# Kernel tuning notes

Hardware: AMD Instinct MI355X
Metric: run time of the kernel (lower is better)

Reference implementation:

```python
import jax, jax.numpy as jnp
import numpy as np

B, T, D = 2, 2048, 2048
NH, HD, R = 16, 128, 64
CQ, CKV = 1536, 512
WINDOW, CHUNK = 512, 256
MIN_SCALE, MAX_SCALE = 0.5, 2.0
ROPE_BASE = 500000.0
EPS = 1e-6


def setup_inputs() -> dict:
    key = jax.random.key(0)
    ks = jax.random.split(key, 12)
    w = lambda k, shape: (jax.random.normal(k, shape, jnp.float32) * 0.02)
    return {
        "x": jax.random.normal(ks[0], (B, T, D), jnp.float32),
        "uncertainty": jax.random.uniform(ks[1], (B, T), jnp.float32),
        "Wq_down": w(ks[2], (D, CQ)),
        "q_norm_w": jnp.ones((CQ,), jnp.float32),
        "Wq_up": w(ks[3], (CQ, NH * HD)),
        "Wq_rope": w(ks[4], (CQ, NH * R)),
        "Wkv_down": w(ks[5], (D, CKV)),
        "kv_norm_w": jnp.ones((CKV,), jnp.float32),
        "Wk_up": w(ks[6], (CKV, NH * HD)),
        "Wv_up": w(ks[7], (CKV, NH * HD)),
        "Wk_rope": w(ks[8], (D, NH * R)),
        "Wout": w(ks[9], (NH * HD, D)),
        "Wgate": w(ks[10], (D, 1)),
        "bgate": jnp.zeros((1,), jnp.float32),
    }


def rms_norm(x, w):
    return x * jax.lax.rsqrt(jnp.mean(x * x, axis=-1, keepdims=True) + EPS) * w


def epe_cos_sin(positions, uncertainty):
    # freq_idx = arange(r//2)*2/r ; theta = base**(-freq_idx)
    half = R // 2
    freq_idx = jnp.arange(half, dtype=jnp.float32) * 2.0 / R
    theta = ROPE_BASE ** (-freq_idx)                                  # [half]
    scale = MIN_SCALE + jnp.clip(uncertainty, 0.0, 1.0) * (MAX_SCALE - MIN_SCALE)  # [B,T]
    freqs = positions[None, :, None].astype(jnp.float32) * theta[None, None, :] * scale[:, :, None]
    freqs = freqs[:, :, None, :]                                      # [B,T,1,half]
    return jnp.cos(freqs), jnp.sin(freqs)


def apply_rope(x, cos, sin):
    # x: [B,T,nH,r]; rotate halves with per-(B,T) cos/sin broadcast over heads
    half = x.shape[-1] // 2
    x1, x2 = x[..., :half], x[..., half:]
    return jnp.concatenate([x1 * cos - x2 * sin, x2 * cos + x1 * sin], axis=-1)


def sliding_window_attn(Q, K, V, window, chunk):
    # Q,K: [B,nH,T,dk], V: [B,nH,T,dv]; chunked causal sliding-window
    b, nh, t, dk = Q.shape
    dv = V.shape[-1]
    half_w = window // 2
    n_chunks = t // chunk                    # T chosen multiple of chunk
    L = chunk + 2 * half_w
    Kp = jnp.pad(K, ((0, 0), (0, 0), (half_w, half_w), (0, 0)))
    Vp = jnp.pad(V, ((0, 0), (0, 0), (half_w, half_w), (0, 0)))
    starts = jnp.arange(n_chunks) * chunk
    idx = starts[:, None] + jnp.arange(L)[None, :]          # [nC,L] into padded axis
    Kw = Kp[:, :, idx]                                       # [B,nH,nC,L,dk]
    Vw = Vp[:, :, idx]                                       # [B,nH,nC,L,dv]
    Qc = Q.reshape(b, nh, n_chunks, chunk, dk)
    scores = jnp.einsum('bhcqd,bhckd->bhcqk', Qc, Kw) / jnp.sqrt(jnp.float32(dk))
    key_pos = idx - half_w                                   # actual key positions [nC,L]
    q_pos = starts[:, None] + jnp.arange(chunk)[None, :]     # [nC,chunk]
    mask = (key_pos[:, None, :] <= q_pos[:, :, None]) & (key_pos[:, None, :] >= 0)
    scores = jnp.where(mask[None, None], scores, -jnp.inf)
    p = jax.nn.softmax(scores, axis=-1)
    out = jnp.einsum('bhcqk,bhckd->bhcqd', p, Vw)
    return out.reshape(b, nh, t, dv)


def reference(x, uncertainty, Wq_down, q_norm_w, Wq_up, Wq_rope,
              Wkv_down, kv_norm_w, Wk_up, Wv_up, Wk_rope, Wout, Wgate, bgate):
    b, t, d = x.shape
    positions = jnp.arange(t)

    q_lat = rms_norm(x @ Wq_down, q_norm_w)                  # [B,T,CQ]
    q_c = (q_lat @ Wq_up).reshape(b, t, NH, HD)
    q_r = (q_lat @ Wq_rope).reshape(b, t, NH, R)
    kv_lat = rms_norm(x @ Wkv_down, kv_norm_w)               # [B,T,CKV]
    k_c = (kv_lat @ Wk_up).reshape(b, t, NH, HD)
    v = (kv_lat @ Wv_up).reshape(b, t, NH, HD)
    k_r = (x @ Wk_rope).reshape(b, t, NH, R)

    cos, sin = epe_cos_sin(positions, uncertainty)
    q_r = apply_rope(q_r, cos, sin)
    k_r = apply_rope(k_r, cos, sin)

    Q = jnp.concatenate([q_c, q_r], axis=-1).transpose(0, 2, 1, 3)   # [B,nH,T,HD+R]
    K = jnp.concatenate([k_c, k_r], axis=-1).transpose(0, 2, 1, 3)
    V = v.transpose(0, 2, 1, 3)                                       # [B,nH,T,HD]

    out_ar = sliding_window_attn(Q, K, V, WINDOW, CHUNK)

    # full bidirectional SDPA
    scale = 1.0 / jnp.sqrt(jnp.float32(HD + R))
    scores = jnp.einsum('bhqd,bhkd->bhqk', Q, K) * scale
    out_bidir = jnp.einsum('bhqk,bhkd->bhqd', jax.nn.softmax(scores, axis=-1), V)

    alpha = jax.nn.sigmoid((x @ Wgate + bgate)).squeeze(-1)           # [B,T]
    a = alpha[:, None, :, None]
    merged = a * out_bidir + (1.0 - a) * out_ar                       # [B,nH,T,HD]
    merged = merged.transpose(0, 2, 1, 3).reshape(b, t, NH * HD)
    return merged @ Wout, alpha
```

## Files before the change

kernel.cpp:

```cpp
#include <hip/hip_runtime.h>
#include <hip/hip_bf16.h>
#include <math.h>

typedef __hip_bfloat16 bf16;
using v8bf = __attribute__((ext_vector_type(8))) __bf16;
using v4f  = __attribute__((ext_vector_type(4))) float;
using f32x16 = __attribute__((ext_vector_type(16))) float;
using v4u = __attribute__((ext_vector_type(4))) unsigned;
using v4s = __attribute__((ext_vector_type(4))) short;
using v8s = __attribute__((ext_vector_type(8))) short;

#define T_SEQ 2048
#define DMODEL 2048
#define NHEADS 16
#define HDIM 128
#define RDIM 64

__device__ __forceinline__ short f2bfbits(float f) {
  bf16 h = __float2bfloat16(f);
  short s;
  __builtin_memcpy(&s, &h, 2);
  return s;
}

__device__ __forceinline__ float bfbits2f(short s) {
  bf16 h;
  __builtin_memcpy(&h, &s, 2);
  return __bfloat162float(h);
}

__device__ __forceinline__ unsigned pk2bf(float a, float b) {
  unsigned lo = (unsigned short)f2bfbits(a);
  unsigned hi = (unsigned short)f2bfbits(b);
  return lo | (hi << 16);
}

typedef const __attribute__((address_space(1))) unsigned gu32;
typedef __attribute__((address_space(3))) unsigned lu32;
__device__ __forceinline__ void gl_lds16(const void* g, void* l) {
  __builtin_amdgcn_global_load_lds((gu32*)g, (lu32*)l, 16, 0, 0);
}

__global__ void detect_k(const unsigned* __restrict__ x, int* __restrict__ flag) {
  __shared__ int cnt;
  if (threadIdx.x == 0) cnt = 0;
  __syncthreads();
  int c = 0;
#pragma unroll
  for (int i = 0; i < 4; i++) {
    unsigned w = x[threadIdx.x * 4 + i];
    unsigned e = (w >> 7) & 0xFFu;
    if (e < 97u || e > 157u) c++;
  }
  atomicAdd(&cnt, c);
  __syncthreads();
  if (threadIdx.x == 0) flag[0] = (cnt > 256) ? 1 : 0;
}

__global__ __launch_bounds__(256) void conv_all(const void* x_raw,
                                                const void* qnw_raw, const void* kvnw_raw,
                                                const void* wg_raw, const void* bg_raw,
                                                const void* unc_raw,
                                                bf16* xc, bf16* qnw, bf16* kvnw,
                                                bf16* wgc, bf16* bgc, float* uncf,
                                                const int* flag) {
  bool isf = (*flag != 0);
  if (blockIdx.x < 32768) {
    int i = blockIdx.x * 256 + threadIdx.x;
    xc[i] = isf ? __float2bfloat16(((const float*)x_raw)[i]) : ((const bf16*)x_raw)[i];
  } else {
    int i = (blockIdx.x - 32768) * 256 + threadIdx.x;
    if (i < 1536) qnw[i] = isf ? __float2bfloat16(((const float*)qnw_raw)[i]) : ((const bf16*)qnw_raw)[i];
    else if (i < 2048) { int j = i - 1536; kvnw[j] = isf ? __float2bfloat16(((const float*)kvnw_raw)[j]) : ((const bf16*)kvnw_raw)[j]; }
    else if (i < 4096) { int j = i - 2048; wgc[j] = isf ? __float2bfloat16(((const float*)wg_raw)[j]) : ((const bf16*)wg_raw)[j]; }
    else if (i < 4097) bgc[0] = isf ? __float2bfloat16(((const float*)bg_raw)[0]) : ((const bf16*)bg_raw)[0];
    else if (i < 8193) { int j = i - 4097; uncf[j] = isf ? ((const float*)unc_raw)[j] : __bfloat162float(((const bf16*)unc_raw)[j]); }
  }
}

struct TP8 {
  const void* s[8];
  bf16* d[8];
  int rows[8];
  int cols[8];
  int pre[9];
};

__global__ __launch_bounds__(256) void transpose_all(TP8 jobs, const int* __restrict__ flag) {
  __shared__ bf16 tile[32][33];
  int bid = blockIdx.x;
  int w = 0;
#pragma unroll
  for (int k = 0; k < 7; k++) if (bid >= jobs.pre[k + 1]) w = k + 1;
  int lt = bid - jobs.pre[w];
  int rows = jobs.rows[w], cols = jobs.cols[w];
  int tpr = cols >> 5;
  int by = (lt / tpr) << 5, bx = (lt % tpr) << 5;
  const void* src = jobs.s[w];
  bf16* dst = jobs.d[w];
  int tx = threadIdx.x & 31, ty = threadIdx.x >> 5;
  bool isf = (*flag != 0);
#pragma unroll
  for (int i = 0; i < 32; i += 8) {
    size_t idx = (size_t)(by + ty + i) * cols + bx + tx;
    tile[ty + i][tx] = isf ? __float2bfloat16(((const float*)src)[idx])
                           : ((const bf16*)src)[idx];
  }
  __syncthreads();
#pragma unroll
  for (int i = 0; i < 32; i += 8)
    dst[(size_t)(bx + ty + i) * rows + by + tx] = tile[tx][ty + i];
}

__global__ __launch_bounds__(256) void transpose_str(const bf16* __restrict__ src,
                                                     bf16* __restrict__ dst,
                                                     int srcStride, int dstStride) {
  __shared__ bf16 tile[32][33];
  int bx = blockIdx.x * 32, by = blockIdx.y * 32;
  int tx = threadIdx.x & 31, ty = threadIdx.x >> 5;
#pragma unroll
  for (int i = 0; i < 32; i += 8)
    tile[ty + i][tx] = src[(size_t)(by + ty + i) * srcStride + bx + tx];
  __syncthreads();
#pragma unroll
  for (int i = 0; i < 32; i += 8)
    dst[(size_t)(bx + ty + i) * dstStride + by + tx] = tile[tx][ty + i];
}

__global__ __launch_bounds__(256) void gemm_tn(const bf16* __restrict__ A,
                                               const bf16* __restrict__ BT,
                                               bf16* __restrict__ Cb,
                                               int M, int N, int K,
                                               const int* __restrict__ oflag,
                                               void* __restrict__ dvout) {
  __shared__ __align__(16) short lsa[128 * 32];
  __shared__ __align__(16) short lsb[128 * 32];
  const int m0 = blockIdx.y * 128, n0 = blockIdx.x * 128;
  const int tid = threadIdx.x;
  const int w = tid >> 6, lane = tid & 63, quad = lane >> 4, l16 = lane & 15;
  const int wm = (w >> 1) * 64, wn = (w & 1) * 64;
  const int srow = ((lane >> 5) & 1) * 8 + (lane & 7);
  const int skq  = (lane >> 3) & 3;
  const int r0 = w * 2, r1 = w * 2 + 1;
  const bf16* Ab0 = A  + (size_t)(m0 + r0 * 16 + srow) * K + skq * 8;
  const bf16* Ab1 = A  + (size_t)(m0 + r1 * 16 + srow) * K + skq * 8;
  const bf16* Bb0 = BT + (size_t)(n0 + r0 * 16 + srow) * K + skq * 8;
  const bf16* Bb1 = BT + (size_t)(n0 + r1 * 16 + srow) * K + skq * 8;
  short* la0 = &lsa[r0 * 512];
  short* la1 = &lsa[r1 * 512];
  short* lb0 = &lsb[r0 * 512];
  short* lb1 = &lsb[r1 * 512];

  v4f acc[4][4];
#pragma unroll
  for (int i = 0; i < 4; i++)
#pragma unroll
    for (int j = 0; j < 4; j++) acc[i][j] = (v4f){0.f, 0.f, 0.f, 0.f};

  for (int kb = 0; kb < K; kb += 32) {
    __syncthreads();
    gl_lds16(Ab0 + kb, la0);
    gl_lds16(Ab1 + kb, la1);
    gl_lds16(Bb0 + kb, lb0);
    gl_lds16(Bb1 + kb, lb1);
    __syncthreads();

    v8bf af[4], bfr[4];
#pragma unroll
    for (int i = 0; i < 4; i++) {
      int row = wm + i * 16 + l16;
      af[i] = *reinterpret_cast<const v8bf*>(
          &lsa[((row >> 3) << 8) + (quad << 6) + ((row & 7) << 3)]);
    }
#pragma unroll
    for (int j = 0; j < 4; j++) {
      int row = wn + j * 16 + l16;
      bfr[j] = *reinterpret_cast<const v8bf*>(
          &lsb[((row >> 3) << 8) + (quad << 6) + ((row & 7) << 3)]);
    }
#pragma unroll
    for (int i = 0; i < 4; i++)
#pragma unroll
      for (int j = 0; j < 4; j++)
        acc[i][j] = __builtin_amdgcn_mfma_f32_16x16x32_bf16(af[i], bfr[j], acc[i][j], 0, 0, 0);
  }
  const bool isf = dvout && (*oflag != 0);
#pragma unroll
  for (int i = 0; i < 4; i++)
#pragma unroll
    for (int j = 0; j < 4; j++)
#pragma unroll
      for (int r = 0; r < 4; r++) {
        int row = m0 + wm + i * 16 + quad * 4 + r;
        int col = n0 + wn + j * 16 + l16;
        float vv = acc[i][j][r];
        size_t idx = (size_t)row * N + col;
        if (dvout) {
          if (isf) ((float*)dvout)[idx] = vv;
          else     ((bf16*)dvout)[idx] = __float2bfloat16(vv);
        } else {
          Cb[idx] = __float2bfloat16(vv);
        }
      }
}

__global__ __launch_bounds__(256) void rmsnorm_both(const bf16* __restrict__ xproj,
                                                    const bf16* __restrict__ qnw,
                                                    const bf16* __restrict__ kvnw,
                                                    bf16* __restrict__ q_lat,
                                                    bf16* __restrict__ kv_lat) {
  int bid = blockIdx.x, tid = threadIdx.x;
  bool isq = bid < 4096;
  int row = isq ? bid : bid - 4096;
  int C = isq ? 1536 : 512;
  const bf16* r = xproj + (size_t)row * 3072 + (isq ? 0 : 1536);
  const bf16* w = isq ? qnw : kvnw;
  bf16* o = (isq ? q_lat : kv_lat) + (size_t)row * C;
  float s = 0.f;
  for (int i = tid; i < C; i += 256) { float v = __bfloat162float(r[i]); s += v * v; }
#pragma unroll
  for (int m = 32; m; m >>= 1) s += __shfl_xor(s, m);
  __shared__ float red[4];
  if ((tid & 63) == 0) red[tid >> 6] = s;
  __syncthreads();
  float tot = red[0] + red[1] + red[2] + red[3];
  float rs = rsqrtf(tot / (float)C + 1e-6f);
  for (int i = tid; i < C; i += 256)
    o[i] = __float2bfloat16(__bfloat162float(r[i]) * rs * __bfloat162float(w[i]));
}

__global__ __launch_bounds__(256) void rope_gate(bf16* __restrict__ qcr,
                                                 bf16* __restrict__ xproj,
                                                 const float* __restrict__ unc,
                                                 const bf16* __restrict__ x,
                                                 const bf16* __restrict__ wg,
                                                 const bf16* __restrict__ bg,
                                                 float* __restrict__ af,
                                                 void* __restrict__ dout,
                                                 const int* __restrict__ flag) {
  __shared__ float red[4];
  int tid = threadIdx.x;
  if (blockIdx.x < 8192) {
    int idx = blockIdx.x * 256 + tid;
    int j = idx & 31, h = (idx >> 5) & 15, bt = idx >> 9;
    int t = bt & (T_SEQ - 1);
    float u = unc[bt];
    u = fminf(fmaxf(u, 0.f), 1.f);
    float scale = 0.5f + 1.5f * u;
    float theta = expf(-(float)j * (1.f / 32.f) * logf(500000.f));
    float f = (float)t * theta * scale;
    float c = cosf(f), s = sinf(f);
    size_t base = (size_t)bt * 3072 + 2048 + h * RDIM + j;
    {
      float x1 = __bfloat162float(qcr[base]), x2 = __bfloat162float(qcr[base + 32]);
      qcr[base]      = __float2bfloat16(x1 * c - x2 * s);
      qcr[base + 32] = __float2bfloat16(x2 * c + x1 * s);
    }
    {
      float x1 = __bfloat162float(xproj[base]), x2 = __bfloat162float(xproj[base + 32]);
      xproj[base]      = __float2bfloat16(x1 * c - x2 * s);
      xproj[base + 32] = __float2bfloat16(x2 * c + x1 * s);
    }
  } else {
    int row = blockIdx.x - 8192;
    const bf16* xr = x + (size_t)row * DMODEL;
    float s = 0.f;
    for (int i = tid; i < DMODEL; i += 256)
      s += __bfloat162float(xr[i]) * __bfloat162float(wg[i]);
#pragma unroll
    for (int m = 32; m; m >>= 1) s += __shfl_xor(s, m);
    if ((tid & 63) == 0) red[tid >> 6] = s;
    __syncthreads();
    if (tid == 0) {
      float tot = red[0] + red[1] + red[2] + red[3] + __bfloat162float(bg[0]);
      float a = 1.f / (1.f + expf(-tot));
      af[row] = a;
      size_t oi = (size_t)8388608 + row;
      if (*flag) ((float*)dout)[oi] = a;
      else       ((bf16*)dout)[oi] = __float2bfloat16(a);
    }
  }
}

__global__ __launch_bounds__(256, 2) void attn_f(const bf16* __restrict__ qcr,
                                                 const bf16* __restrict__ kcv,
                                                 const bf16* __restrict__ xproj,
                                                 const bf16* __restrict__ vt,
                                                 const float* __restrict__ alphaF,
                                                 float* __restrict__ arp,
                                                 bf16* __restrict__ out) {
  constexpr int LDK = 200;
  constexpr int LDV = 72;
  __shared__ __align__(16) short sh[64 * LDK + 128 * LDV];
  short* lk  = sh;
  short* lvt = sh + 64 * LDK;

  const int b = blockIdx.z, h = blockIdx.y, qt = blockIdx.x;
  const int qs = qt * 128;
  const int tid = threadIdx.x;
  const int w = tid >> 6, lane = tid & 63;
  const int l5 = lane & 31, h8 = lane >> 5;
  const int q0 = qs + w * 32;
  const int myq = q0 + l5;

  v8bf qf[12];
  {
    const bf16* qcb = qcr + ((size_t)b * T_SEQ + myq) * 3072 + h * HDIM;
#pragma unroll
    for (int ks = 0; ks < 8; ks++)
      qf[ks] = *reinterpret_cast<const v8bf*>(qcb + ks * 16 + h8 * 8);
    const bf16* qrb = qcr + ((size_t)b * T_SEQ + myq) * 3072 + 2048 + h * RDIM;
#pragma unroll
    for (int ks = 0; ks < 4; ks++)
      qf[8 + ks] = *reinterpret_cast<const v8bf*>(qrb + ks * 16 + h8 * 8);
  }

  float l_sum = 0.f;
  f32x16 oacc[4];
#pragma unroll
  for (int nd = 0; nd < 4; nd++)
#pragma unroll
    for (int r = 0; r < 16; r++) oacc[nd][r] = 0.f;

  const float a_q = alphaF[b * T_SEQ + myq];
  const float sc = 0.07216878364870323f;

  const int c   = qs >> 8;
  const int klo = (c > 0) ? (c * 256 - 256) : 0;
  const int A   = klo >> 6;
  const int n1  = ((qs + 128) >> 6) - A;
  const int diag_idx = n1 - 2 + (w >> 1);

  int koc[4], ldc_[4];
#pragma unroll
  for (int i = 0; i < 4; i++) {
    int cc = i * 256 + tid;
    int row = cc >> 4, dg = cc & 15;
    koc[i]  = row * 4096 + dg * 8;
    ldc_[i] = row * LDK + dg * 8;
  }
  int kor[2], ldr_[2];
#pragma unroll
  for (int i = 0; i < 2; i++) {
    int cc = i * 256 + tid;
    int row = cc >> 3, dg = cc & 7;
    kor[i]  = row * 3072 + dg * 8;
    ldr_[i] = row * LDK + 128 + dg * 8;
  }
  int kov[4], ldv_[4];
#pragma unroll
  for (int i = 0; i < 4; i++) {
    int cc = i * 256 + tid;
    int d = cc >> 3, kg = cc & 7;
    kov[i]  = d * 4096 + kg * 8;
    ldv_[i] = d * LDV + kg * 8;
  }
  const bf16* kc_base = kcv   + (size_t)b * T_SEQ * 4096 + h * HDIM;
  const bf16* kr_base = xproj + (size_t)b * T_SEQ * 3072 + 2048 + h * RDIM;
  const bf16* v_base  = vt    + (size_t)h * HDIM * (2 * T_SEQ) + b * T_SEQ;

  v4u rc[4], rr[2], rv[4];
  auto kb_of = [&](int idx) -> int {
    int t = (idx < n1) ? (A + idx) : ((idx < n1 + A) ? (idx - n1) : idx);
    return t << 6;
  };
  auto issue = [&](int kb) {
    const bf16* pc = kc_base + (size_t)kb * 4096;
    const bf16* pr = kr_base + (size_t)kb * 3072;
    const bf16* pv = v_base + kb;
#pragma unroll
    for (int i = 0; i < 4; i++) rc[i] = *reinterpret_cast<const v4u*>(pc + koc[i]);
#pragma unroll
    for (int i = 0; i < 2; i++) rr[i] = *reinterpret_cast<const v4u*>(pr + kor[i]);
#pragma unroll
    for (int i = 0; i < 4; i++) rv[i] = *reinterpret_cast<const v4u*>(pv + kov[i]);
  };

  auto qk = [&](int j) -> f32x16 {
    f32x16 s;
#pragma unroll
    for (int r = 0; r < 16; r++) s[r] = 0.f;
#pragma unroll
    for (int ks = 0; ks < 12; ks++) {
      v8bf kf = *reinterpret_cast<const v8bf*>(&lk[(j * 32 + l5) * LDK + ks * 16 + h8 * 8]);
      s = __builtin_amdgcn_mfma_f32_32x32x16_bf16(kf, qf[ks], s, 0, 0, 0);
    }
    return s;
  };
  auto packf = [&](const float* p, v8bf* pf) {
#pragma unroll
    for (int cc = 0; cc < 2; cc++) {
      unsigned Y0 = pk2bf(p[cc * 8 + 0], p[cc * 8 + 1]);
      unsigned Y1 = pk2bf(p[cc * 8 + 2], p[cc * 8 + 3]);
      unsigned Y2 = pk2bf(p[cc * 8 + 4], p[cc * 8 + 5]);
      unsigned Y3 = pk2bf(p[cc * 8 + 6], p[cc * 8 + 7]);
      asm volatile("v_permlane32_swap_b32 %0, %1" : "+v"(Y0), "+v"(Y2));
      asm volatile("v_permlane32_swap_b32 %0, %1" : "+v"(Y1), "+v"(Y3));
      v4u t; t.x = Y0; t.y = Y1; t.z = Y2; t.w = Y3;
      pf[cc] = __builtin_bit_cast(v8bf, t);
    }
  };
  auto pvj = [&](int j, const v8bf* pf) {
#pragma unroll
    for (int ck = 0; ck < 2; ck++)
#pragma unroll
      for (int nd = 0; nd < 4; nd++) {
        v8bf vf = *reinterpret_cast<const v8bf*>(&lvt[(nd * 32 + l5) * LDV + (j * 2 + ck) * 16 + h8 * 8]);
        oacc[nd] = __builtin_amdgcn_mfma_f32_32x32x16_bf16(vf, pf[ck], oacc[nd], 0, 0, 0);
      }
  };
  auto plainpass = [&](const f32x16& s, int j) {
    float p[16];
#pragma unroll
    for (int r = 0; r < 16; r++) { float e = __expf(s[r] * sc); p[r] = e; l_sum += e; }
    v8bf pf[2];
    packf(p, pf);
    pvj(j, pf);
  };
  auto maskpass = [&](const f32x16& s, int j, int kb, bool upper) {
    float p[16];
#pragma unroll
    for (int r = 0; r < 16; r++) {
      int kk = kb + j * 32 + (r & 3) + 8 * (r >> 2) + 4 * h8;
      float e = __expf(s[r] * sc);
      bool keep = upper ? (kk > myq) : (kk <= myq);
      e = keep ? e : 0.f;
      p[r] = e;
      l_sum += e;
    }
    v8bf pf[2];
    packf(p, pf);
    pvj(j, pf);
  };

  issue(kb_of(0));

  for (int idx = 0; idx < 32; idx++) {
    const int kb = kb_of(idx);
    __syncthreads();
#pragma unroll
    for (int i = 0; i < 4; i++) *reinterpret_cast<v4u*>(&lk[ldc_[i]]) = rc[i];
#pragma unroll
    for (int i = 0; i < 2; i++) *reinterpret_cast<v4u*>(&lk[ldr_[i]]) = rr[i];
#pragma unroll
    for (int i = 0; i < 4; i++) *reinterpret_cast<v4u*>(&lvt[ldv_[i]]) = rv[i];
    if (idx + 1 < 32) issue(kb_of(idx + 1));
    __syncthreads();

    __builtin_amdgcn_s_setprio(1);
    if (idx != diag_idx) {
      plainpass(qk(0), 0);
      plainpass(qk(1), 1);
    } else {
      f32x16 s0 = qk(0);
      f32x16 s1 = qk(1);
      maskpass(s0, 0, kb, false);
      maskpass(s1, 1, kb, false);
      {
        float lar = l_sum + __shfl_xor(l_sum, 32);
        float invar = (1.f - a_q) / lar;
#pragma unroll
        for (int nd = 0; nd < 4; nd++)
#pragma unroll
          for (int r = 0; r < 16; r++) {
            int d = nd * 32 + (r & 3) + 8 * (r >> 2) + 4 * h8;
            arp[((size_t)((b * NHEADS + h) * HDIM + d)) * T_SEQ + myq] = oacc[nd][r] * invar;
          }
      }
      maskpass(s0, 0, kb, true);
      maskpass(s1, 1, kb, true);
    }
    __builtin_amdgcn_s_setprio(0);
  }

  l_sum += __shfl_xor(l_sum, 32);
  float inv = a_q / l_sum;

  __syncthreads();
  short* tile = sh + w * (32 * 136);
  const float* arpb = arp + (size_t)((b * NHEADS + h) * HDIM) * T_SEQ + myq;
#pragma unroll
  for (int nd = 0; nd < 4; nd++)
#pragma unroll
    for (int rg = 0; rg < 4; rg++) {
      v4s pk;
#pragma unroll
      for (int i = 0; i < 4; i++) {
        int d = nd * 32 + rg * 8 + h8 * 4 + i;
        float val = oacc[nd][rg * 4 + i] * inv + arpb[(size_t)d * T_SEQ];
        pk[i] = f2bfbits(val);
      }
      *reinterpret_cast<v4s*>(&tile[l5 * 136 + nd * 32 + rg * 8 + h8 * 4]) = pk;
    }
  __syncthreads();
#pragma unroll
  for (int i = 0; i < 8; i++) {
    int r = i * 4 + (lane >> 4);
    int q2 = qs + w * 32 + r;
    int dcol = (lane & 15) * 8;
    v8s mv = *reinterpret_cast<const v8s*>(&tile[r * 136 + dcol]);
    size_t gbase = ((size_t)b * T_SEQ + q2) * DMODEL + h * HDIM + dcol;
    *reinterpret_cast<v8s*>((void*)(out + gbase)) = mv;
  }
}

extern "C" void kernel_launch(void* const* d_in, const int* in_sizes, int n_in,
                              void* d_out, int out_size, void* d_ws, size_t ws_size,
                              hipStream_t stream) {
  const void* x_raw    = d_in[0];
  const void* unc_raw  = d_in[1];
  const void* Wqd_raw  = d_in[2];
  const void* qnw_raw  = d_in[3];
  const void* Wqu_raw  = d_in[4];
  const void* Wqr_raw  = d_in[5];
  const void* Wkvd_raw = d_in[6];
  const void* kvnw_raw = d_in[7];
  const void* Wku_raw  = d_in[8];
  const void* Wvu_raw  = d_in[9];
  const void* Wkr_raw  = d_in[10];
  const void* Wo_raw   = d_in[11];
  const void* Wg_raw   = d_in[12];
  const void* bg_raw   = d_in[13];

  char* ws = (char*)d_ws;
  size_t off = 0;
  auto alloc = [&](size_t bytes) -> void* {
    char* p = ws + off;
    off += (bytes + 255) & ~(size_t)255;
    return p;
  };
  int*  flag   = (int*)alloc(256);
  bf16* xc     = (bf16*)alloc((size_t)4096 * 2048 * 2);
  float* uncf  = (float*)alloc((size_t)4096 * 4);
  bf16* qnw    = (bf16*)alloc(1536 * 2);
  bf16* kvnw   = (bf16*)alloc(512 * 2);
  bf16* wgc    = (bf16*)alloc(2048 * 2);
  bf16* bgc    = (bf16*)alloc(256);
  bf16* BT1    = (bf16*)alloc((size_t)3072 * 2048 * 2);
  bf16* BT2    = (bf16*)alloc((size_t)3072 * 1536 * 2);
  bf16* BT3    = (bf16*)alloc((size_t)4096 * 512 * 2);
  bf16* WoT    = (bf16*)alloc((size_t)2048 * 2048 * 2);
  bf16* xproj  = (bf16*)alloc((size_t)4096 * 3072 * 2);
  bf16* q_lat  = (bf16*)alloc((size_t)4096 * 1536 * 2);
  bf16* kv_lat = (bf16*)alloc((size_t)4096 * 512 * 2);
  bf16* qcr    = (bf16*)alloc((size_t)4096 * 3072 * 2);
  bf16* kcv    = (bf16*)alloc((size_t)4096 * 4096 * 2);
  bf16* vT     = (bf16*)alloc((size_t)4096 * 2048 * 2);
  float* arp   = (float*)alloc((size_t)2 * NHEADS * HDIM * T_SEQ * 4);
  bf16* attno  = (bf16*)alloc((size_t)4096 * 2048 * 2);
  float* alphaF= (float*)alloc((size_t)4096 * 4);

  detect_k<<<1, 256, 0, stream>>>((const unsigned*)x_raw, flag);

  conv_all<<<32801, 256, 0, stream>>>(x_raw, qnw_raw, kvnw_raw, Wg_raw, bg_raw, unc_raw,
                                      xc, qnw, kvnw, wgc, bgc, uncf, flag);

  TP8 jobs;
  const void* srcs[8] = {Wqd_raw, Wkvd_raw, Wkr_raw, Wqu_raw, Wqr_raw, Wku_raw, Wvu_raw, Wo_raw};
  bf16* dsts[8] = {BT1, BT1 + (size_t)1536 * 2048, BT1 + (size_t)2048 * 2048,
                   BT2, BT2 + (size_t)2048 * 1536,
                   BT3, BT3 + (size_t)2048 * 512, WoT};
  int rws[8] = {2048, 2048, 2048, 1536, 1536, 512, 512, 2048};
  int cls[8] = {1536, 512, 1024, 2048, 1024, 2048, 2048, 2048};
  int acc_t = 0;
  for (int i = 0; i < 8; i++) {
    jobs.s[i] = srcs[i]; jobs.d[i] = dsts[i];
    jobs.rows[i] = rws[i]; jobs.cols[i] = cls[i];
    jobs.pre[i] = acc_t;
    acc_t += (rws[i] / 32) * (cls[i] / 32);
  }
  jobs.pre[8] = acc_t;
  transpose_all<<<acc_t, 256, 0, stream>>>(jobs, flag);

  auto gemmb = [&](const bf16* A, const bf16* BT, bf16* C, int M, int N, int K) {
    gemm_tn<<<dim3(N / 128, M / 128), 256, 0, stream>>>(A, BT, C, M, N, K, nullptr, nullptr);
  };

  gemmb(xc, BT1, xproj, 4096, 3072, 2048);
  rmsnorm_both<<<8192, 256, 0, stream>>>(xproj, qnw, kvnw, q_lat, kv_lat);
  gemmb(q_lat, BT2, qcr, 4096, 3072, 1536);
  gemmb(kv_lat, BT3, kcv, 4096, 4096, 512);

  transpose_str<<<dim3(64, 128), 256, 0, stream>>>(kcv + 2048, vT, 4096, 4096);

  rope_gate<<<12288, 256, 0, stream>>>(qcr, xproj, uncf, xc, wgc, bgc, alphaF, d_out, flag);

  attn_f<<<dim3(16, 16, 2), 256, 0, stream>>>(qcr, kcv, xproj, vT, alphaF, arp, attno);

  gemm_tn<<<dim3(16, 32), 256, 0, stream>>>(attno, WoT, nullptr, 4096, 2048, 2048, flag, d_out);

  (void)in_sizes; (void)n_in; (void)out_size; (void)ws_size;
}
```

Measured before the change: 679.3 us.

## Keep sliding-window partial in registers via snapshot instead of global scratch

The attention kernel now walks key blocks in natural order and takes a register snapshot of the accumulator and row sum at the window start. At the diagonal it forms the windowed output as a difference from that snapshot, which removes the global arp scratch buffer and its strided writes and reads. Block indices are also remapped so blocks sharing the same batch and head land on the same XCD for L2 reuse. The extra snapshot registers add pressure and may limit occupancy, and subtracting two accumulators adds some rounding error.

```diff
diff --git a/kernel.cpp b/kernel.cpp
--- a/kernel.cpp
+++ b/kernel.cpp
@@ -287,7 +287,6 @@
                                                  const bf16* __restrict__ xproj,
                                                  const bf16* __restrict__ vt,
                                                  const float* __restrict__ alphaF,
-                                                 float* __restrict__ arp,
                                                  bf16* __restrict__ out) {
   constexpr int LDK = 200;
   constexpr int LDV = 72;
@@ -295,7 +294,12 @@
   short* lk  = sh;
   short* lvt = sh + 64 * LDK;
 
-  const int b = blockIdx.z, h = blockIdx.y, qt = blockIdx.x;
+  const int f_ = blockIdx.x;
+  const int xcd = f_ & 7, g_ = f_ >> 3;
+  const int qt = g_ & 15;
+  const int p_ = xcd + 8 * (g_ >> 4);
+  const int h = p_ & 15, b = p_ >> 4;
+
   const int qs = qt * 128;
   const int tid = threadIdx.x;
   const int w = tid >> 6, lane = tid & 63;
@@ -315,65 +319,41 @@
       qf[8 + ks] = *reinterpret_cast<const v8bf*>(qrb + ks * 16 + h8 * 8);
   }
 
-  float l_sum = 0.f;
-  f32x16 oacc[4];
+  float l_sum = 0.f, l_snap = 0.f;
+  f32x16 oacc[4], snap[4];
 #pragma unroll
   for (int nd = 0; nd < 4; nd++)
 #pragma unroll
-    for (int r = 0; r < 16; r++) oacc[nd][r] = 0.f;
+    for (int r = 0; r < 16; r++) { oacc[nd][r] = 0.f; snap[nd][r] = 0.f; }
 
   const float a_q = alphaF[b * T_SEQ + myq];
   const float sc = 0.07216878364870323f;
 
-  const int c   = qs >> 8;
-  const int klo = (c > 0) ? (c * 256 - 256) : 0;
-  const int A   = klo >> 6;
-  const int n1  = ((qs + 128) >> 6) - A;
-  const int diag_idx = n1 - 2 + (w >> 1);
-
-  int koc[4], ldc_[4];
-#pragma unroll
-  for (int i = 0; i < 4; i++) {
-    int cc = i * 256 + tid;
-    int row = cc >> 4, dg = cc & 15;
-    koc[i]  = row * 4096 + dg * 8;
-    ldc_[i] = row * LDK + dg * 8;
-  }
-  int kor[2], ldr_[2];
-#pragma unroll
-  for (int i = 0; i < 2; i++) {
-    int cc = i * 256 + tid;
-    int row = cc >> 3, dg = cc & 7;
-    kor[i]  = row * 3072 + dg * 8;
-    ldr_[i] = row * LDK + 128 + dg * 8;
-  }
-  int kov[4], ldv_[4];
-#pragma unroll
-  for (int i = 0; i < 4; i++) {
-    int cc = i * 256 + tid;
-    int d = cc >> 3, kg = cc & 7;
-    kov[i]  = d * 4096 + kg * 8;
-    ldv_[i] = d * LDV + kg * 8;
-  }
+  const int c_ = qs >> 8;
+  const int klo  = (c_ > 0) ? (c_ * 256 - 256) : 0;
+  const int kb_d = qs + (w >> 1) * 64;
+
+  const int koc0 = (tid >> 4) * 4096 + (tid & 15) * 8;
+  const int ldc0 = (tid >> 4) * LDK  + (tid & 15) * 8;
+  const int kor0 = (tid >> 3) * 3072 + (tid & 7) * 8;
+  const int ldr0 = (tid >> 3) * LDK + 128 + (tid & 7) * 8;
+  const int kov0 = (tid >> 3) * 4096 + (tid & 7) * 8;
+  const int ldv0 = (tid >> 3) * LDV  + (tid & 7) * 8;
   const bf16* kc_base = kcv   + (size_t)b * T_SEQ * 4096 + h * HDIM;
   const bf16* kr_base = xproj + (size_t)b * T_SEQ * 3072 + 2048 + h * RDIM;
   const bf16* v_base  = vt    + (size_t)h * HDIM * (2 * T_SEQ) + b * T_SEQ;
 
   v4u rc[4], rr[2], rv[4];
-  auto kb_of = [&](int idx) -> int {
-    int t = (idx < n1) ? (A + idx) : ((idx < n1 + A) ? (idx - n1) : idx);
-    return t << 6;
-  };
   auto issue = [&](int kb) {
     const bf16* pc = kc_base + (size_t)kb * 4096;
     const bf16* pr = kr_base + (size_t)kb * 3072;
     const bf16* pv = v_base + kb;
 #pragma unroll
-    for (int i = 0; i < 4; i++) rc[i] = *reinterpret_cast<const v4u*>(pc + koc[i]);
-#pragma unroll
-    for (int i = 0; i < 2; i++) rr[i] = *reinterpret_cast<const v4u*>(pr + kor[i]);
-#pragma unroll
-    for (int i = 0; i < 4; i++) rv[i] = *reinterpret_cast<const v4u*>(pv + kov[i]);
+    for (int i = 0; i < 4; i++) rc[i] = *reinterpret_cast<const v4u*>(pc + koc0 + i * 65536);
+#pragma unroll
+    for (int i = 0; i < 2; i++) rr[i] = *reinterpret_cast<const v4u*>(pr + kor0 + i * 98304);
+#pragma unroll
+    for (int i = 0; i < 4; i++) rv[i] = *reinterpret_cast<const v4u*>(pv + kov0 + i * 131072);
   };
 
   auto qk = [&](int j) -> f32x16 {
@@ -387,18 +367,15 @@
     }
     return s;
   };
-  auto packf = [&](const float* p, v8bf* pf) {
-#pragma unroll
-    for (int cc = 0; cc < 2; cc++) {
-      unsigned Y0 = pk2bf(p[cc * 8 + 0], p[cc * 8 + 1]);
-      unsigned Y1 = pk2bf(p[cc * 8 + 2], p[cc * 8 + 3]);
-      unsigned Y2 = pk2bf(p[cc * 8 + 4], p[cc * 8 + 5]);
-      unsigned Y3 = pk2bf(p[cc * 8 + 6], p[cc * 8 + 7]);
-      asm volatile("v_permlane32_swap_b32 %0, %1" : "+v"(Y0), "+v"(Y2));
-      asm volatile("v_permlane32_swap_b32 %0, %1" : "+v"(Y1), "+v"(Y3));
-      v4u t; t.x = Y0; t.y = Y1; t.z = Y2; t.w = Y3;
-      pf[cc] = __builtin_bit_cast(v8bf, t);
-    }
+  auto pack8 = [&](const float* p) -> v8bf {
+    unsigned Y0 = pk2bf(p[0], p[1]);
+    unsigned Y1 = pk2bf(p[2], p[3]);
+    unsigned Y2 = pk2bf(p[4], p[5]);
+    unsigned Y3 = pk2bf(p[6], p[7]);
+    asm volatile("v_permlane32_swap_b32 %0, %1" : "+v"(Y0), "+v"(Y2));
+    asm volatile("v_permlane32_swap_b32 %0, %1" : "+v"(Y1), "+v"(Y3));
+    v4u t; t.x = Y0; t.y = Y1; t.z = Y2; t.w = Y3;
+    return __builtin_bit_cast(v8bf, t);
   };
   auto pvj = [&](int j, const v8bf* pf) {
 #pragma unroll
@@ -409,66 +386,81 @@
         oacc[nd] = __builtin_amdgcn_mfma_f32_32x32x16_bf16(vf, pf[ck], oacc[nd], 0, 0, 0);
       }
   };
-  auto plainpass = [&](const f32x16& s, int j) {
-    float p[16];
-#pragma unroll
-    for (int r = 0; r < 16; r++) { float e = __expf(s[r] * sc); p[r] = e; l_sum += e; }
+  auto plainpass = [&](int j) {
+    f32x16 s = qk(j);
     v8bf pf[2];
-    packf(p, pf);
+#pragma unroll
+    for (int cc = 0; cc < 2; cc++) {
+      float p[8];
+#pragma unroll
+      for (int r8 = 0; r8 < 8; r8++) {
+        float e = __expf(s[cc * 8 + r8] * sc);
+        p[r8] = e;
+        l_sum += e;
+      }
+      pf[cc] = pack8(p);
+    }
     pvj(j, pf);
   };
-  auto maskpass = [&](const f32x16& s, int j, int kb, bool upper) {
-    float p[16];
-#pragma unroll
-    for (int r = 0; r < 16; r++) {
-      int kk = kb + j * 32 + (r & 3) + 8 * (r >> 2) + 4 * h8;
-      float e = __expf(s[r] * sc);
-      bool keep = upper ? (kk > myq) : (kk <= myq);
-      e = keep ? e : 0.f;
-      p[r] = e;
-      l_sum += e;
-    }
+  auto maskpass = [&](int j, int kb, bool upper) {
+    f32x16 s = qk(j);
     v8bf pf[2];
-    packf(p, pf);
+#pragma unroll
+    for (int cc = 0; cc < 2; cc++) {
+      float p[8];
+#pragma unroll
+      for (int r8 = 0; r8 < 8; r8++) {
+        int r = cc * 8 + r8;
+        int kk = kb + j * 32 + (r & 3) + 8 * (r >> 2) + 4 * h8;
+        float e = __expf(s[r] * sc);
+        bool keep = upper ? (kk > myq) : (kk <= myq);
+        e = keep ? e : 0.f;
+        p[r8] = e;
+        l_sum += e;
+      }
+      pf[cc] = pack8(p);
+    }
     pvj(j, pf);
   };
 
-  issue(kb_of(0));
-
-  for (int idx = 0; idx < 32; idx++) {
-    const int kb = kb_of(idx);
+  issue(0);
+
+  for (int kb = 0; kb < T_SEQ; kb += 64) {
     __syncthreads();
 #pragma unroll
-    for (int i = 0; i < 4; i++) *reinterpret_cast<v4u*>(&lk[ldc_[i]]) = rc[i];
-#pragma unroll
-    for (int i = 0; i < 2; i++) *reinterpret_cast<v4u*>(&lk[ldr_[i]]) = rr[i];
-#pragma unroll
-    for (int i = 0; i < 4; i++) *reinterpret_cast<v4u*>(&lvt[ldv_[i]]) = rv[i];
-    if (idx + 1 < 32) issue(kb_of(idx + 1));
+    for (int i = 0; i < 4; i++) *reinterpret_cast<v4u*>(&lk[ldc0 + i * 16 * LDK]) = rc[i];
+#pragma unroll
+    for (int i = 0; i < 2; i++) *reinterpret_cast<v4u*>(&lk[ldr0 + i * 32 * LDK]) = rr[i];
+#pragma unroll
+    for (int i = 0; i < 4; i++) *reinterpret_cast<v4u*>(&lvt[ldv0 + i * 32 * LDV]) = rv[i];
+    if (kb + 64 < T_SEQ) issue(kb + 64);
     __syncthreads();
 
+    if (kb == klo) {
+#pragma unroll
+      for (int nd = 0; nd < 4; nd++) snap[nd] = oacc[nd];
+      l_snap = l_sum;
+    }
+
     __builtin_amdgcn_s_setprio(1);
-    if (idx != diag_idx) {
-      plainpass(qk(0), 0);
-      plainpass(qk(1), 1);
+    if (kb != kb_d) {
+      plainpass(0);
+      plainpass(1);
     } else {
-      f32x16 s0 = qk(0);
-      f32x16 s1 = qk(1);
-      maskpass(s0, 0, kb, false);
-      maskpass(s1, 1, kb, false);
+      maskpass(0, kb, false);
+      maskpass(1, kb, false);
       {
-        float lar = l_sum + __shfl_xor(l_sum, 32);
-        float invar = (1.f - a_q) / lar;
+        float lar_h = l_sum - l_snap;
+        float lar = lar_h + __shfl_xor(lar_h, 32);
+        float sAR = (1.f - a_q) / lar;
 #pragma unroll
         for (int nd = 0; nd < 4; nd++)
 #pragma unroll
-          for (int r = 0; r < 16; r++) {
-            int d = nd * 32 + (r & 3) + 8 * (r >> 2) + 4 * h8;
-            arp[((size_t)((b * NHEADS + h) * HDIM + d)) * T_SEQ + myq] = oacc[nd][r] * invar;
-          }
+          for (int r = 0; r < 16; r++)
+            snap[nd][r] = (oacc[nd][r] - snap[nd][r]) * sAR;
       }
-      maskpass(s0, 0, kb, true);
-      maskpass(s1, 1, kb, true);
+      maskpass(0, kb, true);
+      maskpass(1, kb, true);
     }
     __builtin_amdgcn_s_setprio(0);
   }
@@ -478,7 +470,6 @@
 
   __syncthreads();
   short* tile = sh + w * (32 * 136);
-  const float* arpb = arp + (size_t)((b * NHEADS + h) * HDIM) * T_SEQ + myq;
 #pragma unroll
   for (int nd = 0; nd < 4; nd++)
 #pragma unroll
@@ -486,8 +477,7 @@
       v4s pk;
 #pragma unroll
       for (int i = 0; i < 4; i++) {
-        int d = nd * 32 + rg * 8 + h8 * 4 + i;
-        float val = oacc[nd][rg * 4 + i] * inv + arpb[(size_t)d * T_SEQ];
+        float val = oacc[nd][rg * 4 + i] * inv + snap[nd][rg * 4 + i];
         pk[i] = f2bfbits(val);
       }
       *reinterpret_cast<v4s*>(&tile[l5 * 136 + nd * 32 + rg * 8 + h8 * 4]) = pk;
@@ -546,7 +536,6 @@
   bf16* qcr    = (bf16*)alloc((size_t)4096 * 3072 * 2);
   bf16* kcv    = (bf16*)alloc((size_t)4096 * 4096 * 2);
   bf16* vT     = (bf16*)alloc((size_t)4096 * 2048 * 2);
-  float* arp   = (float*)alloc((size_t)2 * NHEADS * HDIM * T_SEQ * 4);
   bf16* attno  = (bf16*)alloc((size_t)4096 * 2048 * 2);
   float* alphaF= (float*)alloc((size_t)4096 * 4);
 
@@ -585,7 +574,7 @@
 
   rope_gate<<<12288, 256, 0, stream>>>(qcr, xproj, uncf, xc, wgc, bgc, alphaF, d_out, flag);
 
-  attn_f<<<dim3(16, 16, 2), 256, 0, stream>>>(qcr, kcv, xproj, vT, alphaF, arp, attno);
+  attn_f<<<512, 256, 0, stream>>>(qcr, kcv, xproj, vT, alphaF, attno);
 
   gemm_tn<<<dim3(16, 32), 256, 0, stream>>>(attno, WoT, nullptr, 4096, 2048, 2048, flag, d_out);
 
```

Result: slower. 733.5 us (+8.0%).
